# Kernel optimization log

Measured on AMD Instinct MI355X. Metric: run time of the kernel, lower is better.

Reference implementation:

```python
import jax, jax.numpy as jnp
import numpy as np

N, E, IN_DIM, HID, HEADS, LAYERS, NTYPES, NGRAPH = 50000, 600000, 64, 128, 8, 3, 10, 500
C = HID // HEADS
NEG_SLOPE = 0.2
EPS = 1e-5


def setup_inputs() -> dict:
    key = jax.random.key(0)
    ks = jax.random.split(key, 24)
    inp = {
        "x": jax.random.normal(ks[0], (N, IN_DIM), jnp.float32),
        "edge_index": jax.random.randint(ks[1], (2, E), 0, N),
        "node_types": jax.random.randint(ks[2], (N,), 0, NTYPES),
        "batch": jnp.sort(jax.random.randint(ks[3], (N,), 0, NGRAPH)),
        # node embedding linear
        "emb_W": jax.random.normal(ks[4], (IN_DIM, HID), jnp.float32) / np.sqrt(IN_DIM),
        "emb_b": jnp.zeros((HID,), jnp.float32),
        "ntype_emb": jax.random.normal(ks[5], (NTYPES, HID), jnp.float32) * 0.02,
        # stacked GAT layer params
        "gat_W": jax.random.normal(ks[6], (LAYERS, HID, HID), jnp.float32) / np.sqrt(HID),
        "att_src": jax.random.normal(ks[7], (LAYERS, HEADS, C), jnp.float32) * 0.1,
        "att_dst": jax.random.normal(ks[8], (LAYERS, HEADS, C), jnp.float32) * 0.1,
        "gat_b": jnp.zeros((LAYERS, HID), jnp.float32),
        "ln_g": jnp.ones((LAYERS, HID), jnp.float32),
        "ln_b": jnp.zeros((LAYERS, HID), jnp.float32),
        # global attention MLP
        "ga_W1": jax.random.normal(ks[9], (HID, HID), jnp.float32) / np.sqrt(HID),
        "ga_b1": jnp.zeros((HID,), jnp.float32),
        "ga_W2": jax.random.normal(ks[10], (HID, 1), jnp.float32) / np.sqrt(HID),
        "ga_b2": jnp.zeros((1,), jnp.float32),
        # graph classifier head
        "cls_W1": jax.random.normal(ks[11], (HID, HID), jnp.float32) / np.sqrt(HID),
        "cls_b1": jnp.zeros((HID,), jnp.float32),
        "cls_W2": jax.random.normal(ks[12], (HID, 1), jnp.float32) / np.sqrt(HID),
        "cls_b2": jnp.zeros((1,), jnp.float32),
    }
    return inp


def _layer_norm(h, g, b):
    mu = jnp.mean(h, axis=-1, keepdims=True)
    var = jnp.mean(jnp.square(h - mu), axis=-1, keepdims=True)
    return (h - mu) * jax.lax.rsqrt(var + EPS) * g + b


def _gat_layer(h, src, dst, W, a_src, a_dst, bias):
    # h: [N, HID] -> per-head projection [N, H, C]
    hp = (h @ W).reshape(N, HEADS, C)
    alpha_s = jnp.sum(hp * a_src, axis=-1)  # [N, H]
    alpha_d = jnp.sum(hp * a_dst, axis=-1)  # [N, H]
    e = jax.nn.leaky_relu(alpha_s[src] + alpha_d[dst], NEG_SLOPE)  # [E', H]
    # segment softmax over incoming edges of each destination node
    m = jax.ops.segment_max(e, dst, num_segments=N)
    ex = jnp.exp(e - m[dst])
    s = jax.ops.segment_sum(ex, dst, num_segments=N)
    alpha = ex / s[dst]  # every node has a self-loop, so s > 0
    msg = hp[src] * alpha[:, :, None]  # [E', H, C]
    out = jax.ops.segment_sum(msg, dst, num_segments=N)  # [N, H, C]
    return out.reshape(N, HID) + bias


def reference(x, edge_index, node_types, batch, emb_W, emb_b, ntype_emb,
              gat_W, att_src, att_dst, gat_b, ln_g, ln_b,
              ga_W1, ga_b1, ga_W2, ga_b2, cls_W1, cls_b1, cls_W2, cls_b2):
    # self-loops (PyG GATConv add_self_loops=True)
    loop = jnp.arange(N)
    src = jnp.concatenate([edge_index[0], loop])
    dst = jnp.concatenate([edge_index[1], loop])

    h = x @ emb_W + emb_b
    h = h + ntype_emb[node_types]

    for l in range(LAYERS):
        h_prev = h
        h = _gat_layer(h, src, dst, gat_W[l], att_src[l], att_dst[l], gat_b[l])
        h = _layer_norm(h, ln_g[l], ln_b[l])
        h = jax.nn.relu(h + h_prev)

    # global attention pooling: softmax over all nodes (dim 0, as in source)
    scores = jnp.tanh(h @ ga_W1 + ga_b1) @ ga_W2 + ga_b2  # [N, 1]
    attw = jax.nn.softmax(scores, axis=0)
    h_graph = jnp.sum(h * attw, axis=0)  # [HID]

    # global mean pool per graph
    sums = jax.ops.segment_sum(h, batch, num_segments=NGRAPH)  # [G, HID]
    cnts = jax.ops.segment_sum(jnp.ones((N, 1), h.dtype), batch, num_segments=NGRAPH)
    mean_pool = sums / jnp.maximum(cnts, 1.0)

    hg = h_graph + mean_pool  # broadcast [HID] + [G, HID]

    # graph classifier head (features_batch=None path), squeeze(-1)
    out = jax.nn.relu(hg @ cls_W1 + cls_b1) @ cls_W2 + cls_b2
    return out.squeeze(-1)  # [G]
```

## Files before the change

### kernel.cpp

```cpp
#include <hip/hip_runtime.h>
#include <hip/hip_bf16.h>
#include <math.h>

#define HID 128
#define HEADS 8
#define INDIM 64

typedef _Float16 f16x8 __attribute__((ext_vector_type(8)));
typedef _Float16 f16x4 __attribute__((ext_vector_type(4)));
typedef _Float16 f16x2 __attribute__((ext_vector_type(2)));
typedef float f32x4 __attribute__((ext_vector_type(4)));

__device__ __forceinline__ float fast_tanh(float x) {
    return 1.f - 2.f / (__expf(2.f * x) + 1.f);
}

#if defined(__has_builtin)
#if __has_builtin(__builtin_amdgcn_fdot2)
#define HAVE_FDOT2 1
#endif
#endif

__global__ void prologue_kernel(const int* __restrict__ ei, int* __restrict__ deg,
                                const float* __restrict__ emb_W, const float* __restrict__ gat_W,
                                const float* __restrict__ ga_W1, _Float16* __restrict__ wt_emb,
                                _Float16* __restrict__ wt_gat, _Float16* __restrict__ wt_ga1,
                                const int* __restrict__ batch, int* __restrict__ gstart,
                                float* __restrict__ hgZ,
                                int E, int EE, int N, int G) {
    int i = blockIdx.x * blockDim.x + threadIdx.x;
    if (i < EE) {
        int dst = (i < E) ? ei[E + i] : (i - E);
        atomicAdd(&deg[dst], 1);
    }
    if (i < 8192) {
        int k = i >> 7, n = i & 127;
        wt_emb[n * 64 + k] = (_Float16)emb_W[i];
    } else if (i < 8192 + 49152) {
        int j = i - 8192;
        int l = j >> 14, r = j & 16383;
        int k = r >> 7, n = r & 127;
        wt_gat[l * 16384 + n * 128 + k] = (_Float16)gat_W[j];
    } else if (i < 73728) {
        int j = i - 57344;
        int k = j >> 7, n = j & 127;
        wt_ga1[n * 128 + k] = (_Float16)ga_W1[j];
    } else if (i < 73728 + 129) {
        hgZ[i - 73728] = 0.f;
    }
    if (i >= 100000 && i - 100000 <= G) {
        int g = i - 100000;
        int lo = 0, hi = N;
        while (lo < hi) {
            int mid = (lo + hi) >> 1;
            if (batch[mid] < g) lo = mid + 1; else hi = mid;
        }
        gstart[g] = lo;
    }
}

__global__ __launch_bounds__(256) void mfma_proj_kernel(
    int mode, int K, int N,
    const _Float16* __restrict__ A16, const float* __restrict__ Af32,
    const _Float16* __restrict__ Wt,
    const float* __restrict__ bias, const float* __restrict__ nemb,
    const int* __restrict__ ntypes, _Float16* __restrict__ h16out,
    const float* __restrict__ asrc, const float* __restrict__ adst,
    _Float16* __restrict__ hp_out, float* __restrict__ als, float* __restrict__ ald,
    const float* __restrict__ w2, const float* __restrict__ b2,
    float* __restrict__ escore,
    int PB, int task, const int* __restrict__ ei2,
    const int* __restrict__ degc,
    int* __restrict__ rowptrw, int* __restrict__ woffw, int* __restrict__ esrcw,
    int E2, int EE2)
{
    __shared__ _Float16 w_lds[128 * 136];
    __shared__ _Float16 a_lds[64 * 136];
    int t = threadIdx.x;

    if ((int)blockIdx.x >= PB) {
        if (task == 1) {
            int b = (int)blockIdx.x - PB;
            int i = b * 256 + t;
            int v = (i < N) ? degc[i] : 0;
            int pe = 0;
            for (int j = t; j < (b << 8); j += 256) pe += degc[j];
#pragma unroll
            for (int m = 32; m >= 1; m >>= 1) pe += __shfl_xor(pe, m, 64);
            int* itmp  = (int*)a_lds;
            int* itmp2 = itmp + 256;
            itmp[t] = v;
            if ((t & 63) == 0) itmp2[t >> 6] = pe;
            __syncthreads();
#pragma unroll
            for (int off = 1; off < 256; off <<= 1) {
                int x = (t >= off) ? itmp[t - off] : 0;
                __syncthreads();
                itmp[t] += x;
                __syncthreads();
            }
            pe = itmp2[0] + itmp2[1] + itmp2[2] + itmp2[3];
            int excl = itmp[t] - v + pe;
            if (i < N) { rowptrw[i] = excl; woffw[i] = excl; }
            if (b == 0 && t == 0) rowptrw[N] = EE2;
        } else {
            int sb = (int)blockIdx.x - PB;
            int stride = ((int)gridDim.x - PB) << 8;
            for (int e = sb * 256 + t; e < EE2; e += stride) {
                int src, dst;
                if (e < E2) { src = ei2[e]; dst = ei2[E2 + e]; } else { src = dst = e - E2; }
                int slot = atomicAdd(&woffw[dst], 1);
                esrcw[slot] = src;
            }
        }
        return;
    }

    int KP = K + 8;
    int K8 = K >> 3;

    for (int i = t; i < 128 * K8; i += 256) {
        int row = i / K8, c8 = i - row * K8;
        *(f16x8*)&w_lds[row * KP + 8 * c8] = *(const f16x8*)&Wt[(size_t)row * K + 8 * c8];
    }

    int lane = t & 63, wv = t >> 6;
    int l15 = lane & 15, quad = lane >> 4;

    for (int tile = 0; tile < 2; ++tile) {
        int n0 = blockIdx.x * 128 + tile * 64;
        if (n0 >= N) break;
        __syncthreads();
        if (mode == 0) {
            for (int i = t; i < 64 * K8; i += 256) {
                int row = i / K8, c8 = i - row * K8;
                f16x8 v = {};
                int n = n0 + row;
                if (n < N) {
                    const float4* p = (const float4*)&Af32[(size_t)n * K + 8 * c8];
                    float4 a = p[0], b = p[1];
                    v[0] = (_Float16)a.x; v[1] = (_Float16)a.y;
                    v[2] = (_Float16)a.z; v[3] = (_Float16)a.w;
                    v[4] = (_Float16)b.x; v[5] = (_Float16)b.y;
                    v[6] = (_Float16)b.z; v[7] = (_Float16)b.w;
                }
                *(f16x8*)&a_lds[row * KP + 8 * c8] = v;
            }
        } else {
            for (int i = t; i < 64 * K8; i += 256) {
                int row = i / K8, c8 = i - row * K8;
                f16x8 v = {};
                if (n0 + row < N) v = *(const f16x8*)&A16[(size_t)(n0 + row) * K + 8 * c8];
                *(f16x8*)&a_lds[row * KP + 8 * c8] = v;
            }
        }
        __syncthreads();

        f32x4 acc[8];
#pragma unroll
        for (int c = 0; c < 8; ++c) acc[c] = (f32x4){0.f, 0.f, 0.f, 0.f};

        int ksteps = K >> 5;
        for (int kk = 0; kk < ksteps; ++kk) {
            f16x8 af = *(const f16x8*)&a_lds[(wv * 16 + l15) * KP + kk * 32 + quad * 8];
#pragma unroll
            for (int c = 0; c < 8; ++c) {
                f16x8 bf = *(const f16x8*)&w_lds[(c * 16 + l15) * KP + kk * 32 + quad * 8];
                acc[c] = __builtin_amdgcn_mfma_f32_16x16x32_f16(af, bf, acc[c], 0, 0, 0);
            }
        }

        if (mode == 0) {
            float bv[8];
#pragma unroll
            for (int c = 0; c < 8; ++c) bv[c] = bias[c * 16 + l15];
            __syncthreads();
#pragma unroll
            for (int r = 0; r < 4; ++r) {
                int n = n0 + wv * 16 + quad * 4 + r;
                int nt = (n < N) ? ntypes[n] : 0;
#pragma unroll
                for (int c = 0; c < 8; ++c)
                    a_lds[(wv * 16 + quad * 4 + r) * 136 + c * 16 + l15] =
                        (_Float16)(acc[c][r] + bv[c] + nemb[nt * HID + c * 16 + l15]);
            }
            __syncthreads();
            for (int i = t; i < 64 * 16; i += 256) {
                int row = i >> 4, c8 = i & 15;
                int n = n0 + row;
                if (n < N) *(f16x8*)&h16out[(size_t)n * HID + 8 * c8] = *(const f16x8*)&a_lds[row * 136 + 8 * c8];
            }
        } else if (mode == 1) {
            __syncthreads();
#pragma unroll
            for (int c = 0; c < 8; ++c)
#pragma unroll
                for (int r = 0; r < 4; ++r)
                    a_lds[(wv * 16 + quad * 4 + r) * 136 + c * 16 + l15] = (_Float16)acc[c][r];
            __syncthreads();
            for (int i = t; i < 64 * 16; i += 256) {
                int row = i >> 4, c8 = i & 15;
                int n = n0 + row;
                if (n < N) *(f16x8*)&hp_out[(size_t)n * HID + 8 * c8] = *(const f16x8*)&a_lds[row * 136 + 8 * c8];
            }
            for (int task2 = t; task2 < 512; task2 += 256) {
                int row = task2 >> 3, hd = task2 & 7;
                int n = n0 + row;
                if (n >= N) continue;
                f16x8 v0 = *(const f16x8*)&a_lds[row * 136 + hd * 16];
                f16x8 v1 = *(const f16x8*)&a_lds[row * 136 + hd * 16 + 8];
                float va = 0.f, vd = 0.f;
#pragma unroll
                for (int j = 0; j < 8; ++j) {
                    va += (float)v0[j] * asrc[hd * 16 + j] + (float)v1[j] * asrc[hd * 16 + 8 + j];
                    vd += (float)v0[j] * adst[hd * 16 + j] + (float)v1[j] * adst[hd * 16 + 8 + j];
                }
                als[n * HEADS + hd] = va;
                ald[n * HEADS + hd] = vd;
            }
        } else {
            float b2v = b2[0];
            float treg[4] = {0.f, 0.f, 0.f, 0.f};
#pragma unroll
            for (int c = 0; c < 8; ++c) {
                float b1v = bias[c * 16 + l15];
                float w2v = w2[c * 16 + l15];
#pragma unroll
                for (int r = 0; r < 4; ++r)
                    treg[r] += fast_tanh(acc[c][r] + b1v) * w2v;
            }
#pragma unroll
            for (int r = 0; r < 4; ++r) {
                float v = treg[r];
#pragma unroll
                for (int m = 8; m >= 1; m >>= 1) v += __shfl_xor(v, m, 64);
                if (l15 == 0) {
                    int n = n0 + wv * 16 + quad * 4 + r;
                    if (n < N) escore[n] = __expf(v + b2v);
                }
            }
        }
    }
}

__global__ void gat_aggregate_kernel(const int* __restrict__ rowptr, const int* __restrict__ esrc,
                                     const float* __restrict__ als, const float* __restrict__ ald,
                                     const _Float16* __restrict__ hp16, const float* __restrict__ gb,
                                     const float* __restrict__ lg, const float* __restrict__ lb,
                                     _Float16* __restrict__ h16, int N) {
    int wave = threadIdx.x >> 6;
    int lane = threadIdx.x & 63;
    int n = blockIdx.x * 4 + wave;
    if (n >= N) return;
    int esub = lane >> 4;
    int cg = lane & 15;
    int hd = cg >> 1;
    float adv = ald[n * HEADS + hd];
    int row = rowptr[n], end = rowptr[n + 1];
    int last = end - 1;
    float acc[8] = {0.f, 0.f, 0.f, 0.f, 0.f, 0.f, 0.f, 0.f};
    float sw = 0.f;
    for (int base = row; base < end; base += 16) {
        int iA = base + esub;
        int iB = iA + 4, iC = iA + 8, iD = iA + 12;
        int cA = iA <= last ? iA : last;
        int cB = iB <= last ? iB : last;
        int cC = iC <= last ? iC : last;
        int cD = iD <= last ? iD : last;
        int sA = esrc[cA], sB = esrc[cB], sC = esrc[cC], sD = esrc[cD];
        f16x8 pA = *(const f16x8*)&hp16[(size_t)sA * HID + cg * 8];
        f16x8 pB = *(const f16x8*)&hp16[(size_t)sB * HID + cg * 8];
        f16x8 pC = *(const f16x8*)&hp16[(size_t)sC * HID + cg * 8];
        f16x8 pD = *(const f16x8*)&hp16[(size_t)sD * HID + cg * 8];
        float aA = als[sA * HEADS + hd];
        float aB = als[sB * HEADS + hd];
        float aC = als[sC * HEADS + hd];
        float aD = als[sD * HEADS + hd];
        float lA = aA + adv; lA = lA > 0.f ? lA : 0.2f * lA;
        float lB = aB + adv; lB = lB > 0.f ? lB : 0.2f * lB;
        float lC = aC + adv; lC = lC > 0.f ? lC : 0.2f * lC;
        float lD = aD + adv; lD = lD > 0.f ? lD : 0.2f * lD;
        float wA = __expf(lA) * ((iA < end) ? 1.f : 0.f);
        float wB = __expf(lB) * ((iB < end) ? 1.f : 0.f);
        float wC = __expf(lC) * ((iC < end) ? 1.f : 0.f);
        float wD = __expf(lD) * ((iD < end) ? 1.f : 0.f);
        sw += (wA + wB) + (wC + wD);
#ifdef HAVE_FDOT2
        f16x2 wAB; wAB[0] = (_Float16)wA; wAB[1] = (_Float16)wB;
        f16x2 wCD; wCD[0] = (_Float16)wC; wCD[1] = (_Float16)wD;
#pragma unroll
        for (int j = 0; j < 8; ++j) {
            f16x2 prAB; prAB[0] = pA[j]; prAB[1] = pB[j];
            f16x2 prCD; prCD[0] = pC[j]; prCD[1] = pD[j];
            acc[j] = __builtin_amdgcn_fdot2(prAB, wAB, acc[j], false);
            acc[j] = __builtin_amdgcn_fdot2(prCD, wCD, acc[j], false);
        }
#else
#pragma unroll
        for (int j = 0; j < 8; ++j)
            acc[j] += wA * (float)pA[j] + wB * (float)pB[j]
                    + wC * (float)pC[j] + wD * (float)pD[j];
#endif
    }
#pragma unroll
    for (int m = 16; m <= 32; m <<= 1) {
        sw += __shfl_xor(sw, m, 64);
#pragma unroll
        for (int j = 0; j < 8; ++j) acc[j] += __shfl_xor(acc[j], m, 64);
    }
    float inv_sw = 1.f / sw;
    float4 g0 = ((const float4*)(gb + cg * 8))[0];
    float4 g1 = ((const float4*)(gb + cg * 8))[1];
    float v[8];
    v[0] = acc[0] * inv_sw + g0.x; v[1] = acc[1] * inv_sw + g0.y;
    v[2] = acc[2] * inv_sw + g0.z; v[3] = acc[3] * inv_sw + g0.w;
    v[4] = acc[4] * inv_sw + g1.x; v[5] = acc[5] * inv_sw + g1.y;
    v[6] = acc[6] * inv_sw + g1.z; v[7] = acc[7] * inv_sw + g1.w;
    float s = 0.f;
#pragma unroll
    for (int j = 0; j < 8; ++j) s += v[j];
#pragma unroll
    for (int m = 32; m >= 1; m >>= 1) s += __shfl_xor(s, m, 64);
    float mu = s * (1.f / 512.f);
    float d[8], sq = 0.f;
#pragma unroll
    for (int j = 0; j < 8; ++j) { d[j] = v[j] - mu; sq += d[j] * d[j]; }
#pragma unroll
    for (int m = 32; m >= 1; m >>= 1) sq += __shfl_xor(sq, m, 64);
    float inv = rsqrtf(sq * (1.f / 512.f) + 1e-5f);
    float4 lg0 = ((const float4*)(lg + cg * 8))[0];
    float4 lg1 = ((const float4*)(lg + cg * 8))[1];
    float4 lb0 = ((const float4*)(lb + cg * 8))[0];
    float4 lb1 = ((const float4*)(lb + cg * 8))[1];
    float lgv[8] = {lg0.x, lg0.y, lg0.z, lg0.w, lg1.x, lg1.y, lg1.z, lg1.w};
    float lbv[8] = {lb0.x, lb0.y, lb0.z, lb0.w, lb1.x, lb1.y, lb1.z, lb1.w};
    f16x8 hold = *(const f16x8*)&h16[(size_t)n * HID + cg * 8];
    f16x8 hnew;
#pragma unroll
    for (int j = 0; j < 8; ++j) {
        float r = d[j] * inv * lgv[j] + lbv[j] + (float)hold[j];
        hnew[j] = (_Float16)(r > 0.f ? r : 0.f);
    }
    if (esub == 0) *(f16x8*)&h16[(size_t)n * HID + cg * 8] = hnew;
}

__global__ void pool_graph_kernel(const _Float16* __restrict__ h16, const float* __restrict__ escore,
                                  const int* __restrict__ gstart, float* __restrict__ sums,
                                  float* __restrict__ cnts, float* __restrict__ hgZ, int G) {
    int g = blockIdx.x;
    int t = threadIdx.x;
    int c = t & 127, grp = t >> 7;
    int s = gstart[g], e = gstart[g + 1];
    float msum = 0.f, asum = 0.f, z = 0.f;
    for (int n = s + grp; n < e; n += 4) {
        float hv = (float)h16[(size_t)n * HID + c];
        float es = escore[n];
        msum += hv;
        asum += es * hv;
        if (c == 0) z += es;
    }
    __shared__ float sm[4][HID];
    __shared__ float sa[4][HID];
    __shared__ float sz[4];
    sm[grp][c] = msum;
    sa[grp][c] = asum;
    if (c == 0) sz[grp] = z;
    __syncthreads();
    if (t < HID) {
        float m = sm[0][t] + sm[1][t] + sm[2][t] + sm[3][t];
        float a = sa[0][t] + sa[1][t] + sa[2][t] + sa[3][t];
        sums[(size_t)g * HID + t] = m;
        atomicAdd(&hgZ[t], a);
    } else if (t == HID) {
        cnts[g] = (float)(e - s);
        atomicAdd(&hgZ[HID], sz[0] + sz[1] + sz[2] + sz[3]);
    }
}

__global__ void head_kernel(const float* __restrict__ hgZ, const float* __restrict__ sums,
                            const float* __restrict__ cnts, const float* __restrict__ W1,
                            const float* __restrict__ b1, const float* __restrict__ W2,
                            const float* __restrict__ b2, float* __restrict__ out, int G) {
    int g = blockIdx.x;
    int t = threadIdx.x;
    __shared__ float hr[HID];
    __shared__ float part[2];
    float Z = hgZ[HID];
    float cnt = cnts[g];
    cnt = cnt > 1.f ? cnt : 1.f;
    hr[t] = hgZ[t] / Z + sums[(size_t)g * HID + t] / cnt;
    __syncthreads();
    float acc = b1[t];
#pragma unroll 8
    for (int k = 0; k < HID; ++k) acc += hr[k] * W1[k * HID + t];
    acc = acc > 0.f ? acc : 0.f;
    float v = acc * W2[t];
#pragma unroll
    for (int m = 32; m >= 1; m >>= 1) v += __shfl_xor(v, m, 64);
    if ((t & 63) == 0) part[t >> 6] = v;
    __syncthreads();
    if (t == 0) out[g] = part[0] + part[1] + b2[0];
}

extern "C" void kernel_launch(void* const* d_in, const int* in_sizes, int n_in,
                              void* d_out, int out_size, void* d_ws, size_t ws_size,
                              hipStream_t stream) {
    const float* x        = (const float*)d_in[0];
    const int*   ei       = (const int*)d_in[1];
    const int*   ntypes   = (const int*)d_in[2];
    const int*   batch    = (const int*)d_in[3];
    const float* emb_W    = (const float*)d_in[4];
    const float* emb_b    = (const float*)d_in[5];
    const float* nemb     = (const float*)d_in[6];
    const float* gat_W    = (const float*)d_in[7];
    const float* att_src  = (const float*)d_in[8];
    const float* att_dst  = (const float*)d_in[9];
    const float* gat_b    = (const float*)d_in[10];
    const float* ln_g     = (const float*)d_in[11];
    const float* ln_b     = (const float*)d_in[12];
    const float* ga_W1    = (const float*)d_in[13];
    const float* ga_b1    = (const float*)d_in[14];
    const float* ga_W2    = (const float*)d_in[15];
    const float* ga_b2    = (const float*)d_in[16];
    const float* cls_W1   = (const float*)d_in[17];
    const float* cls_b1   = (const float*)d_in[18];
    const float* cls_W2   = (const float*)d_in[19];
    const float* cls_b2   = (const float*)d_in[20];
    float* out = (float*)d_out;

    const int N  = in_sizes[2];
    const int E  = in_sizes[1] / 2;
    const int EE = E + N;
    const int G  = out_size;
    const int NB = (N + 255) / 256;

    float* ws      = (float*)d_ws;
    float* als     = ws;
    float* ald     = als + (size_t)N * HEADS;
    float* escore  = ald + (size_t)N * HEADS;
    float* sums    = escore + N;
    float* cnts    = sums + (size_t)G * HID;
    float* hgZ     = cnts + G;
    _Float16* h16  = (_Float16*)(hgZ + HID + 1);
    _Float16* hp16 = h16 + (size_t)N * HID;
    _Float16* wt_emb = hp16 + (size_t)N * HID;
    _Float16* wt_gat = wt_emb + 128 * 64;
    _Float16* wt_ga1 = wt_gat + 3 * 128 * 128;
    int*   rowptr  = (int*)(wt_ga1 + 128 * 128);
    int*   woff    = rowptr + (N + 1);
    int*   deg     = woff + N;
    int*   esrc    = deg + N;
    int*   gstart  = esrc + EE;

    hipMemsetAsync(deg, 0, (size_t)N * sizeof(int), stream);
    int ptot = EE;
    if (ptot < 100000 + G + 1) ptot = 100000 + G + 1;
    prologue_kernel<<<(ptot + 255) / 256, 256, 0, stream>>>(
        ei, deg, emb_W, gat_W, ga_W1, wt_emb, wt_gat, wt_ga1,
        batch, gstart, hgZ, E, EE, N, G);

    const int PB = (N + 127) / 128;
    int SCB = 768 - PB;
    if (SCB < 128) SCB = 128;

    mfma_proj_kernel<<<PB + NB, 256, 0, stream>>>(
        0, INDIM, N, nullptr, x, wt_emb, emb_b, nemb, ntypes, h16,
        nullptr, nullptr, nullptr, nullptr, nullptr, nullptr, nullptr, nullptr,
        PB, 1, nullptr, deg, rowptr, woff, nullptr, E, EE);

    mfma_proj_kernel<<<PB + SCB, 256, 0, stream>>>(
        1, HID, N, h16, nullptr, wt_gat,
        nullptr, nullptr, nullptr, nullptr,
        att_src, att_dst, hp16, als, ald, nullptr, nullptr, nullptr,
        PB, 2, ei, nullptr, nullptr, woff, esrc, E, EE);

    gat_aggregate_kernel<<<(N + 3) / 4, 256, 0, stream>>>(
        rowptr, esrc, als, ald, hp16,
        gat_b, ln_g, ln_b, h16, N);

    for (int l = 1; l < 3; ++l) {
        mfma_proj_kernel<<<PB, 256, 0, stream>>>(
            1, HID, N, h16, nullptr, wt_gat + (size_t)l * HID * HID,
            nullptr, nullptr, nullptr, nullptr,
            att_src + l * HID, att_dst + l * HID,
            hp16, als, ald, nullptr, nullptr, nullptr,
            PB, 0, nullptr, nullptr, nullptr, nullptr, nullptr, 0, 0);
        gat_aggregate_kernel<<<(N + 3) / 4, 256, 0, stream>>>(
            rowptr, esrc, als, ald, hp16,
            gat_b + l * HID, ln_g + l * HID, ln_b + l * HID, h16, N);
    }

    mfma_proj_kernel<<<PB, 256, 0, stream>>>(
        2, HID, N, h16, nullptr, wt_ga1, ga_b1, nullptr, nullptr, nullptr,
        nullptr, nullptr, nullptr, nullptr, nullptr, ga_W2, ga_b2, escore,
        PB, 0, nullptr, nullptr, nullptr, nullptr, nullptr, 0, 0);

    pool_graph_kernel<<<G, 512, 0, stream>>>(h16, escore, gstart, sums, cnts, hgZ, G);
    head_kernel<<<G, 128, 0, stream>>>(hgZ, sums, cnts, cls_W1, cls_b1, cls_W2, cls_b2, out, G);
}
```

Measured before the change: 403.7 us.

## Fuse GAT aggregation with next-layer projection and merge embedding with layer-0 projection

Each layer's aggregate/LayerNorm/residual stage now writes its output rows into LDS and immediately runs the next layer's MFMA projection, or the final attention-score MLP, in the same kernel. The projected features and attention logits ping-pong between two buffers so no layer overwrites what it is still reading. The embedding kernel also computes layer 0's projection, and the CSR scan and scatter run in one launch, with the scatter blocks spin-waiting on a global counter until every scan block is done. This removes several launches and the re-read of h between aggregation and projection. The cost is tiles shrinking from 128 to 64 nodes, more workspace, and a grid-wide spin wait that can deadlock if the scan blocks are not all resident at once.

```diff
diff --git a/kernel.cpp b/kernel.cpp
--- a/kernel.cpp
+++ b/kernel.cpp
@@ -7,7 +7,6 @@
 #define INDIM 64
 
 typedef _Float16 f16x8 __attribute__((ext_vector_type(8)));
-typedef _Float16 f16x4 __attribute__((ext_vector_type(4)));
 typedef _Float16 f16x2 __attribute__((ext_vector_type(2)));
 typedef float f32x4 __attribute__((ext_vector_type(4)));
 
@@ -59,289 +58,346 @@
     }
 }
 
-__global__ __launch_bounds__(256) void mfma_proj_kernel(
-    int mode, int K, int N,
-    const _Float16* __restrict__ A16, const float* __restrict__ Af32,
-    const _Float16* __restrict__ Wt,
-    const float* __restrict__ bias, const float* __restrict__ nemb,
-    const int* __restrict__ ntypes, _Float16* __restrict__ h16out,
+__global__ __launch_bounds__(256) void emb_l0_kernel(
+    const float* __restrict__ x, const _Float16* __restrict__ wt_emb,
+    const float* __restrict__ emb_b, const float* __restrict__ nemb,
+    const int* __restrict__ ntypes,
+    _Float16* __restrict__ h16,
+    const _Float16* __restrict__ wt_g0,
     const float* __restrict__ asrc, const float* __restrict__ adst,
-    _Float16* __restrict__ hp_out, float* __restrict__ als, float* __restrict__ ald,
-    const float* __restrict__ w2, const float* __restrict__ b2,
-    float* __restrict__ escore,
-    int PB, int task, const int* __restrict__ ei2,
-    const int* __restrict__ degc,
-    int* __restrict__ rowptrw, int* __restrict__ woffw, int* __restrict__ esrcw,
-    int E2, int EE2)
+    _Float16* __restrict__ hp_out, float* __restrict__ als_out, float* __restrict__ ald_out,
+    int PB, const int* __restrict__ ei, const int* __restrict__ deg,
+    int* __restrict__ rowptr, int* __restrict__ woff, int* __restrict__ esrc,
+    int* __restrict__ ctr,
+    int N, int E, int EE, int NB)
 {
     __shared__ _Float16 w_lds[128 * 136];
     __shared__ _Float16 a_lds[64 * 136];
     int t = threadIdx.x;
 
     if ((int)blockIdx.x >= PB) {
-        if (task == 1) {
-            int b = (int)blockIdx.x - PB;
-            int i = b * 256 + t;
-            int v = (i < N) ? degc[i] : 0;
-            int pe = 0;
-            for (int j = t; j < (b << 8); j += 256) pe += degc[j];
-#pragma unroll
-            for (int m = 32; m >= 1; m >>= 1) pe += __shfl_xor(pe, m, 64);
-            int* itmp  = (int*)a_lds;
-            int* itmp2 = itmp + 256;
-            itmp[t] = v;
-            if ((t & 63) == 0) itmp2[t >> 6] = pe;
+        int b = (int)blockIdx.x - PB;
+        int i = b * 256 + t;
+        int v = (i < N) ? deg[i] : 0;
+        int pe = 0;
+        for (int j = t; j < (b << 8); j += 256) pe += deg[j];
+#pragma unroll
+        for (int m = 32; m >= 1; m >>= 1) pe += __shfl_xor(pe, m, 64);
+        int* itmp  = (int*)a_lds;
+        int* itmp2 = itmp + 256;
+        itmp[t] = v;
+        if ((t & 63) == 0) itmp2[t >> 6] = pe;
+        __syncthreads();
+#pragma unroll
+        for (int off = 1; off < 256; off <<= 1) {
+            int xx = (t >= off) ? itmp[t - off] : 0;
             __syncthreads();
-#pragma unroll
-            for (int off = 1; off < 256; off <<= 1) {
-                int x = (t >= off) ? itmp[t - off] : 0;
-                __syncthreads();
-                itmp[t] += x;
-                __syncthreads();
-            }
-            pe = itmp2[0] + itmp2[1] + itmp2[2] + itmp2[3];
-            int excl = itmp[t] - v + pe;
-            if (i < N) { rowptrw[i] = excl; woffw[i] = excl; }
-            if (b == 0 && t == 0) rowptrw[N] = EE2;
-        } else {
-            int sb = (int)blockIdx.x - PB;
-            int stride = ((int)gridDim.x - PB) << 8;
-            for (int e = sb * 256 + t; e < EE2; e += stride) {
-                int src, dst;
-                if (e < E2) { src = ei2[e]; dst = ei2[E2 + e]; } else { src = dst = e - E2; }
-                int slot = atomicAdd(&woffw[dst], 1);
-                esrcw[slot] = src;
-            }
+            itmp[t] += xx;
+            __syncthreads();
+        }
+        pe = itmp2[0] + itmp2[1] + itmp2[2] + itmp2[3];
+        int excl = itmp[t] - v + pe;
+        if (i < N) { rowptr[i] = excl; woff[i] = excl; }
+        if (b == 0 && t == 0) rowptr[N] = EE;
+        __threadfence();
+        __syncthreads();
+        if (t == 0) {
+            atomicAdd(ctr, 1);
+            while (atomicAdd(ctr, 0) < NB) __builtin_amdgcn_s_sleep(16);
+        }
+        __syncthreads();
+        for (int e = b * 256 + t; e < EE; e += NB * 256) {
+            int src, dst;
+            if (e < E) { src = ei[e]; dst = ei[E + e]; } else { src = dst = e - E; }
+            int slot = atomicAdd(&woff[dst], 1);
+            esrc[slot] = src;
         }
         return;
     }
 
-    int KP = K + 8;
-    int K8 = K >> 3;
-
-    for (int i = t; i < 128 * K8; i += 256) {
-        int row = i / K8, c8 = i - row * K8;
-        *(f16x8*)&w_lds[row * KP + 8 * c8] = *(const f16x8*)&Wt[(size_t)row * K + 8 * c8];
-    }
+    for (int i = t; i < 128 * 8; i += 256) {
+        int row = i >> 3, c8 = i & 7;
+        *(f16x8*)&w_lds[row * 72 + 8 * c8] = *(const f16x8*)&wt_emb[(size_t)row * 64 + 8 * c8];
+    }
+    int n0 = blockIdx.x * 64;
+    for (int i = t; i < 64 * 8; i += 256) {
+        int row = i >> 3, c8 = i & 7;
+        f16x8 v = {};
+        int n = n0 + row;
+        if (n < N) {
+            const float4* ptr = (const float4*)&x[(size_t)n * 64 + 8 * c8];
+            float4 a = ptr[0], b4 = ptr[1];
+            v[0] = (_Float16)a.x; v[1] = (_Float16)a.y;
+            v[2] = (_Float16)a.z; v[3] = (_Float16)a.w;
+            v[4] = (_Float16)b4.x; v[5] = (_Float16)b4.y;
+            v[6] = (_Float16)b4.z; v[7] = (_Float16)b4.w;
+        }
+        *(f16x8*)&a_lds[row * 72 + 8 * c8] = v;
+    }
+    __syncthreads();
 
     int lane = t & 63, wv = t >> 6;
     int l15 = lane & 15, quad = lane >> 4;
 
-    for (int tile = 0; tile < 2; ++tile) {
-        int n0 = blockIdx.x * 128 + tile * 64;
-        if (n0 >= N) break;
+    f32x4 acc[8];
+#pragma unroll
+    for (int c = 0; c < 8; ++c) acc[c] = (f32x4){0.f, 0.f, 0.f, 0.f};
+#pragma unroll
+    for (int kk = 0; kk < 2; ++kk) {
+        f16x8 af = *(const f16x8*)&a_lds[(wv * 16 + l15) * 72 + kk * 32 + quad * 8];
+#pragma unroll
+        for (int c = 0; c < 8; ++c) {
+            f16x8 bf = *(const f16x8*)&w_lds[(c * 16 + l15) * 72 + kk * 32 + quad * 8];
+            acc[c] = __builtin_amdgcn_mfma_f32_16x16x32_f16(af, bf, acc[c], 0, 0, 0);
+        }
+    }
+    float bv[8];
+#pragma unroll
+    for (int c = 0; c < 8; ++c) bv[c] = emb_b[c * 16 + l15];
+    __syncthreads();
+#pragma unroll
+    for (int r = 0; r < 4; ++r) {
+        int n = n0 + wv * 16 + quad * 4 + r;
+        int nt = (n < N) ? ntypes[n] : 0;
+#pragma unroll
+        for (int c = 0; c < 8; ++c)
+            a_lds[(wv * 16 + quad * 4 + r) * 136 + c * 16 + l15] =
+                (_Float16)(acc[c][r] + bv[c] + nemb[nt * HID + c * 16 + l15]);
+    }
+    for (int i = t; i < 128 * 16; i += 256) {
+        int row = i >> 4, c8 = i & 15;
+        *(f16x8*)&w_lds[row * 136 + 8 * c8] = *(const f16x8*)&wt_g0[(size_t)row * 128 + 8 * c8];
+    }
+    __syncthreads();
+    for (int i = t; i < 64 * 16; i += 256) {
+        int row = i >> 4, c8 = i & 15;
+        int n = n0 + row;
+        if (n < N) *(f16x8*)&h16[(size_t)n * HID + 8 * c8] = *(const f16x8*)&a_lds[row * 136 + 8 * c8];
+    }
+#pragma unroll
+    for (int c = 0; c < 8; ++c) acc[c] = (f32x4){0.f, 0.f, 0.f, 0.f};
+#pragma unroll
+    for (int kk = 0; kk < 4; ++kk) {
+        f16x8 af = *(const f16x8*)&a_lds[(wv * 16 + l15) * 136 + kk * 32 + quad * 8];
+#pragma unroll
+        for (int c = 0; c < 8; ++c) {
+            f16x8 bf = *(const f16x8*)&w_lds[(c * 16 + l15) * 136 + kk * 32 + quad * 8];
+            acc[c] = __builtin_amdgcn_mfma_f32_16x16x32_f16(af, bf, acc[c], 0, 0, 0);
+        }
+    }
+    __syncthreads();
+#pragma unroll
+    for (int c = 0; c < 8; ++c)
+#pragma unroll
+        for (int r = 0; r < 4; ++r)
+            a_lds[(wv * 16 + quad * 4 + r) * 136 + c * 16 + l15] = (_Float16)acc[c][r];
+    __syncthreads();
+    for (int i = t; i < 64 * 16; i += 256) {
+        int row = i >> 4, c8 = i & 15;
+        int n = n0 + row;
+        if (n < N) *(f16x8*)&hp_out[(size_t)n * HID + 8 * c8] = *(const f16x8*)&a_lds[row * 136 + 8 * c8];
+    }
+    for (int task2 = t; task2 < 512; task2 += 256) {
+        int row = task2 >> 3, hd = task2 & 7;
+        int n = n0 + row;
+        if (n >= N) continue;
+        f16x8 v0 = *(const f16x8*)&a_lds[row * 136 + hd * 16];
+        f16x8 v1 = *(const f16x8*)&a_lds[row * 136 + hd * 16 + 8];
+        float va = 0.f, vd = 0.f;
+#pragma unroll
+        for (int j = 0; j < 8; ++j) {
+            va += (float)v0[j] * asrc[hd * 16 + j] + (float)v1[j] * asrc[hd * 16 + 8 + j];
+            vd += (float)v0[j] * adst[hd * 16 + j] + (float)v1[j] * adst[hd * 16 + 8 + j];
+        }
+        als_out[n * HEADS + hd] = va;
+        ald_out[n * HEADS + hd] = vd;
+    }
+}
+
+__global__ __launch_bounds__(256) void fused_agg_proj_kernel(
+    int mode,
+    const int* __restrict__ rowptr, const int* __restrict__ esrc,
+    const float* __restrict__ als_in, const float* __restrict__ ald_in,
+    const _Float16* __restrict__ hp_in,
+    const float* __restrict__ gb, const float* __restrict__ lg, const float* __restrict__ lb,
+    _Float16* __restrict__ h16,
+    const _Float16* __restrict__ Wt,
+    const float* __restrict__ asrc, const float* __restrict__ adst,
+    _Float16* __restrict__ hp_out, float* __restrict__ als_out, float* __restrict__ ald_out,
+    const float* __restrict__ b1, const float* __restrict__ w2, const float* __restrict__ b2,
+    float* __restrict__ escore, int N)
+{
+    __shared__ _Float16 w_lds[128 * 136];
+    __shared__ _Float16 a_lds[64 * 136];
+    int t = threadIdx.x;
+    for (int i = t; i < 128 * 16; i += 256) {
+        int row = i >> 4, c8 = i & 15;
+        *(f16x8*)&w_lds[row * 136 + 8 * c8] = *(const f16x8*)&Wt[(size_t)row * 128 + 8 * c8];
+    }
+    int wave = t >> 6, lane = t & 63;
+    int esub = lane >> 4, cg_ = lane & 15, hd = cg_ >> 1;
+    int n0 = blockIdx.x * 64;
+
+    for (int it = 0; it < 16; ++it) {
+        int n = n0 + wave * 16 + it;
+        if (n >= N) break;
+        float adv = ald_in[n * HEADS + hd];
+        int rs = rowptr[n], re = rowptr[n + 1];
+        int last = re - 1;
+        float acc[8] = {0.f, 0.f, 0.f, 0.f, 0.f, 0.f, 0.f, 0.f};
+        float sw = 0.f;
+        for (int base = rs; base < re; base += 16) {
+            int iA = base + esub;
+            int iB = iA + 4, iC = iA + 8, iD = iA + 12;
+            int cA = iA <= last ? iA : last;
+            int cB = iB <= last ? iB : last;
+            int cC = iC <= last ? iC : last;
+            int cD = iD <= last ? iD : last;
+            int sA = esrc[cA], sB = esrc[cB], sC = esrc[cC], sD = esrc[cD];
+            f16x8 pA = *(const f16x8*)&hp_in[(size_t)sA * HID + cg_ * 8];
+            f16x8 pB = *(const f16x8*)&hp_in[(size_t)sB * HID + cg_ * 8];
+            f16x8 pC = *(const f16x8*)&hp_in[(size_t)sC * HID + cg_ * 8];
+            f16x8 pD = *(const f16x8*)&hp_in[(size_t)sD * HID + cg_ * 8];
+            float aA = als_in[sA * HEADS + hd];
+            float aB = als_in[sB * HEADS + hd];
+            float aC = als_in[sC * HEADS + hd];
+            float aD = als_in[sD * HEADS + hd];
+            float lA = aA + adv; lA = lA > 0.f ? lA : 0.2f * lA;
+            float lB = aB + adv; lB = lB > 0.f ? lB : 0.2f * lB;
+            float lC = aC + adv; lC = lC > 0.f ? lC : 0.2f * lC;
+            float lD = aD + adv; lD = lD > 0.f ? lD : 0.2f * lD;
+            float wA = __expf(lA) * ((iA < re) ? 1.f : 0.f);
+            float wB = __expf(lB) * ((iB < re) ? 1.f : 0.f);
+            float wC = __expf(lC) * ((iC < re) ? 1.f : 0.f);
+            float wD = __expf(lD) * ((iD < re) ? 1.f : 0.f);
+            sw += (wA + wB) + (wC + wD);
+#ifdef HAVE_FDOT2
+            f16x2 wAB; wAB[0] = (_Float16)wA; wAB[1] = (_Float16)wB;
+            f16x2 wCD; wCD[0] = (_Float16)wC; wCD[1] = (_Float16)wD;
+#pragma unroll
+            for (int j = 0; j < 8; ++j) {
+                f16x2 prAB; prAB[0] = pA[j]; prAB[1] = pB[j];
+                f16x2 prCD; prCD[0] = pC[j]; prCD[1] = pD[j];
+                acc[j] = __builtin_amdgcn_fdot2(prAB, wAB, acc[j], false);
+                acc[j] = __builtin_amdgcn_fdot2(prCD, wCD, acc[j], false);
+            }
+#else
+#pragma unroll
+            for (int j = 0; j < 8; ++j)
+                acc[j] += wA * (float)pA[j] + wB * (float)pB[j]
+                        + wC * (float)pC[j] + wD * (float)pD[j];
+#endif
+        }
+#pragma unroll
+        for (int m = 16; m <= 32; m <<= 1) {
+            sw += __shfl_xor(sw, m, 64);
+#pragma unroll
+            for (int j = 0; j < 8; ++j) acc[j] += __shfl_xor(acc[j], m, 64);
+        }
+        float inv_sw = 1.f / sw;
+        float4 g0 = ((const float4*)(gb + cg_ * 8))[0];
+        float4 g1 = ((const float4*)(gb + cg_ * 8))[1];
+        float v[8];
+        v[0] = acc[0] * inv_sw + g0.x; v[1] = acc[1] * inv_sw + g0.y;
+        v[2] = acc[2] * inv_sw + g0.z; v[3] = acc[3] * inv_sw + g0.w;
+        v[4] = acc[4] * inv_sw + g1.x; v[5] = acc[5] * inv_sw + g1.y;
+        v[6] = acc[6] * inv_sw + g1.z; v[7] = acc[7] * inv_sw + g1.w;
+        float s = 0.f;
+#pragma unroll
+        for (int j = 0; j < 8; ++j) s += v[j];
+#pragma unroll
+        for (int m = 32; m >= 1; m >>= 1) s += __shfl_xor(s, m, 64);
+        float mu = s * (1.f / 512.f);
+        float d[8], sq = 0.f;
+#pragma unroll
+        for (int j = 0; j < 8; ++j) { d[j] = v[j] - mu; sq += d[j] * d[j]; }
+#pragma unroll
+        for (int m = 32; m >= 1; m >>= 1) sq += __shfl_xor(sq, m, 64);
+        float inv = rsqrtf(sq * (1.f / 512.f) + 1e-5f);
+        float4 lg0 = ((const float4*)(lg + cg_ * 8))[0];
+        float4 lg1 = ((const float4*)(lg + cg_ * 8))[1];
+        float4 lb0 = ((const float4*)(lb + cg_ * 8))[0];
+        float4 lb1 = ((const float4*)(lb + cg_ * 8))[1];
+        float lgv[8] = {lg0.x, lg0.y, lg0.z, lg0.w, lg1.x, lg1.y, lg1.z, lg1.w};
+        float lbv[8] = {lb0.x, lb0.y, lb0.z, lb0.w, lb1.x, lb1.y, lb1.z, lb1.w};
+        f16x8 hold = *(const f16x8*)&h16[(size_t)n * HID + cg_ * 8];
+        f16x8 hnew;
+#pragma unroll
+        for (int j = 0; j < 8; ++j) {
+            float r = d[j] * inv * lgv[j] + lbv[j] + (float)hold[j];
+            hnew[j] = (_Float16)(r > 0.f ? r : 0.f);
+        }
+        if (esub == 0) {
+            *(f16x8*)&a_lds[(wave * 16 + it) * 136 + cg_ * 8] = hnew;
+            *(f16x8*)&h16[(size_t)n * HID + cg_ * 8] = hnew;
+        }
+    }
+    __syncthreads();
+
+    int l15 = lane & 15, quad = lane >> 4;
+    f32x4 pacc[8];
+#pragma unroll
+    for (int c = 0; c < 8; ++c) pacc[c] = (f32x4){0.f, 0.f, 0.f, 0.f};
+#pragma unroll
+    for (int kk = 0; kk < 4; ++kk) {
+        f16x8 af = *(const f16x8*)&a_lds[(wave * 16 + l15) * 136 + kk * 32 + quad * 8];
+#pragma unroll
+        for (int c = 0; c < 8; ++c) {
+            f16x8 bf = *(const f16x8*)&w_lds[(c * 16 + l15) * 136 + kk * 32 + quad * 8];
+            pacc[c] = __builtin_amdgcn_mfma_f32_16x16x32_f16(af, bf, pacc[c], 0, 0, 0);
+        }
+    }
+
+    if (mode == 1) {
         __syncthreads();
-        if (mode == 0) {
-            for (int i = t; i < 64 * K8; i += 256) {
-                int row = i / K8, c8 = i - row * K8;
-                f16x8 v = {};
-                int n = n0 + row;
-                if (n < N) {
-                    const float4* p = (const float4*)&Af32[(size_t)n * K + 8 * c8];
-                    float4 a = p[0], b = p[1];
-                    v[0] = (_Float16)a.x; v[1] = (_Float16)a.y;
-                    v[2] = (_Float16)a.z; v[3] = (_Float16)a.w;
-                    v[4] = (_Float16)b.x; v[5] = (_Float16)b.y;
-                    v[6] = (_Float16)b.z; v[7] = (_Float16)b.w;
-                }
-                *(f16x8*)&a_lds[row * KP + 8 * c8] = v;
+#pragma unroll
+        for (int c = 0; c < 8; ++c)
+#pragma unroll
+            for (int r = 0; r < 4; ++r)
+                a_lds[(wave * 16 + quad * 4 + r) * 136 + c * 16 + l15] = (_Float16)pacc[c][r];
+        __syncthreads();
+        for (int i = t; i < 64 * 16; i += 256) {
+            int row = i >> 4, c8 = i & 15;
+            int n = n0 + row;
+            if (n < N) *(f16x8*)&hp_out[(size_t)n * HID + 8 * c8] = *(const f16x8*)&a_lds[row * 136 + 8 * c8];
+        }
+        for (int task2 = t; task2 < 512; task2 += 256) {
+            int row = task2 >> 3, hh = task2 & 7;
+            int n = n0 + row;
+            if (n >= N) continue;
+            f16x8 v0 = *(const f16x8*)&a_lds[row * 136 + hh * 16];
+            f16x8 v1 = *(const f16x8*)&a_lds[row * 136 + hh * 16 + 8];
+            float va = 0.f, vd = 0.f;
+#pragma unroll
+            for (int j = 0; j < 8; ++j) {
+                va += (float)v0[j] * asrc[hh * 16 + j] + (float)v1[j] * asrc[hh * 16 + 8 + j];
+                vd += (float)v0[j] * adst[hh * 16 + j] + (float)v1[j] * adst[hh * 16 + 8 + j];
             }
-        } else {
-            for (int i = t; i < 64 * K8; i += 256) {
-                int row = i / K8, c8 = i - row * K8;
-                f16x8 v = {};
-                if (n0 + row < N) v = *(const f16x8*)&A16[(size_t)(n0 + row) * K + 8 * c8];
-                *(f16x8*)&a_lds[row * KP + 8 * c8] = v;
+            als_out[n * HEADS + hh] = va;
+            ald_out[n * HEADS + hh] = vd;
+        }
+    } else {
+        float b2v = b2[0];
+        float treg[4] = {0.f, 0.f, 0.f, 0.f};
+#pragma unroll
+        for (int c = 0; c < 8; ++c) {
+            float b1v = b1[c * 16 + l15];
+            float w2v = w2[c * 16 + l15];
+#pragma unroll
+            for (int r = 0; r < 4; ++r)
+                treg[r] += fast_tanh(pacc[c][r] + b1v) * w2v;
+        }
+#pragma unroll
+        for (int r = 0; r < 4; ++r) {
+            float v = treg[r];
+#pragma unroll
+            for (int m = 8; m >= 1; m >>= 1) v += __shfl_xor(v, m, 64);
+            if (l15 == 0) {
+                int n = n0 + wave * 16 + quad * 4 + r;
+                if (n < N) escore[n] = __expf(v + b2v);
             }
         }
-        __syncthreads();
-
-        f32x4 acc[8];
-#pragma unroll
-        for (int c = 0; c < 8; ++c) acc[c] = (f32x4){0.f, 0.f, 0.f, 0.f};
-
-        int ksteps = K >> 5;
-        for (int kk = 0; kk < ksteps; ++kk) {
-            f16x8 af = *(const f16x8*)&a_lds[(wv * 16 + l15) * KP + kk * 32 + quad * 8];
-#pragma unroll
-            for (int c = 0; c < 8; ++c) {
-                f16x8 bf = *(const f16x8*)&w_lds[(c * 16 + l15) * KP + kk * 32 + quad * 8];
-                acc[c] = __builtin_amdgcn_mfma_f32_16x16x32_f16(af, bf, acc[c], 0, 0, 0);
-            }
-        }
-
-        if (mode == 0) {
-            float bv[8];
-#pragma unroll
-            for (int c = 0; c < 8; ++c) bv[c] = bias[c * 16 + l15];
-            __syncthreads();
-#pragma unroll
-            for (int r = 0; r < 4; ++r) {
-                int n = n0 + wv * 16 + quad * 4 + r;
-                int nt = (n < N) ? ntypes[n] : 0;
-#pragma unroll
-                for (int c = 0; c < 8; ++c)
-                    a_lds[(wv * 16 + quad * 4 + r) * 136 + c * 16 + l15] =
-                        (_Float16)(acc[c][r] + bv[c] + nemb[nt * HID + c * 16 + l15]);
-            }
-            __syncthreads();
-            for (int i = t; i < 64 * 16; i += 256) {
-                int row = i >> 4, c8 = i & 15;
-                int n = n0 + row;
-                if (n < N) *(f16x8*)&h16out[(size_t)n * HID + 8 * c8] = *(const f16x8*)&a_lds[row * 136 + 8 * c8];
-            }
-        } else if (mode == 1) {
-            __syncthreads();
-#pragma unroll
-            for (int c = 0; c < 8; ++c)
-#pragma unroll
-                for (int r = 0; r < 4; ++r)
-                    a_lds[(wv * 16 + quad * 4 + r) * 136 + c * 16 + l15] = (_Float16)acc[c][r];
-            __syncthreads();
-            for (int i = t; i < 64 * 16; i += 256) {
-                int row = i >> 4, c8 = i & 15;
-                int n = n0 + row;
-                if (n < N) *(f16x8*)&hp_out[(size_t)n * HID + 8 * c8] = *(const f16x8*)&a_lds[row * 136 + 8 * c8];
-            }
-            for (int task2 = t; task2 < 512; task2 += 256) {
-                int row = task2 >> 3, hd = task2 & 7;
-                int n = n0 + row;
-                if (n >= N) continue;
-                f16x8 v0 = *(const f16x8*)&a_lds[row * 136 + hd * 16];
-                f16x8 v1 = *(const f16x8*)&a_lds[row * 136 + hd * 16 + 8];
-                float va = 0.f, vd = 0.f;
-#pragma unroll
-                for (int j = 0; j < 8; ++j) {
-                    va += (float)v0[j] * asrc[hd * 16 + j] + (float)v1[j] * asrc[hd * 16 + 8 + j];
-                    vd += (float)v0[j] * adst[hd * 16 + j] + (float)v1[j] * adst[hd * 16 + 8 + j];
-                }
-                als[n * HEADS + hd] = va;
-                ald[n * HEADS + hd] = vd;
-            }
-        } else {
-            float b2v = b2[0];
-            float treg[4] = {0.f, 0.f, 0.f, 0.f};
-#pragma unroll
-            for (int c = 0; c < 8; ++c) {
-                float b1v = bias[c * 16 + l15];
-                float w2v = w2[c * 16 + l15];
-#pragma unroll
-                for (int r = 0; r < 4; ++r)
-                    treg[r] += fast_tanh(acc[c][r] + b1v) * w2v;
-            }
-#pragma unroll
-            for (int r = 0; r < 4; ++r) {
-                float v = treg[r];
-#pragma unroll
-                for (int m = 8; m >= 1; m >>= 1) v += __shfl_xor(v, m, 64);
-                if (l15 == 0) {
-                    int n = n0 + wv * 16 + quad * 4 + r;
-                    if (n < N) escore[n] = __expf(v + b2v);
-                }
-            }
-        }
-    }
-}
-
-__global__ void gat_aggregate_kernel(const int* __restrict__ rowptr, const int* __restrict__ esrc,
-                                     const float* __restrict__ als, const float* __restrict__ ald,
-                                     const _Float16* __restrict__ hp16, const float* __restrict__ gb,
-                                     const float* __restrict__ lg, const float* __restrict__ lb,
-                                     _Float16* __restrict__ h16, int N) {
-    int wave = threadIdx.x >> 6;
-    int lane = threadIdx.x & 63;
-    int n = blockIdx.x * 4 + wave;
-    if (n >= N) return;
-    int esub = lane >> 4;
-    int cg = lane & 15;
-    int hd = cg >> 1;
-    float adv = ald[n * HEADS + hd];
-    int row = rowptr[n], end = rowptr[n + 1];
-    int last = end - 1;
-    float acc[8] = {0.f, 0.f, 0.f, 0.f, 0.f, 0.f, 0.f, 0.f};
-    float sw = 0.f;
-    for (int base = row; base < end; base += 16) {
-        int iA = base + esub;
-        int iB = iA + 4, iC = iA + 8, iD = iA + 12;
-        int cA = iA <= last ? iA : last;
-        int cB = iB <= last ? iB : last;
-        int cC = iC <= last ? iC : last;
-        int cD = iD <= last ? iD : last;
-        int sA = esrc[cA], sB = esrc[cB], sC = esrc[cC], sD = esrc[cD];
-        f16x8 pA = *(const f16x8*)&hp16[(size_t)sA * HID + cg * 8];
-        f16x8 pB = *(const f16x8*)&hp16[(size_t)sB * HID + cg * 8];
-        f16x8 pC = *(const f16x8*)&hp16[(size_t)sC * HID + cg * 8];
-        f16x8 pD = *(const f16x8*)&hp16[(size_t)sD * HID + cg * 8];
-        float aA = als[sA * HEADS + hd];
-        float aB = als[sB * HEADS + hd];
-        float aC = als[sC * HEADS + hd];
-        float aD = als[sD * HEADS + hd];
-        float lA = aA + adv; lA = lA > 0.f ? lA : 0.2f * lA;
-        float lB = aB + adv; lB = lB > 0.f ? lB : 0.2f * lB;
-        float lC = aC + adv; lC = lC > 0.f ? lC : 0.2f * lC;
-        float lD = aD + adv; lD = lD > 0.f ? lD : 0.2f * lD;
-        float wA = __expf(lA) * ((iA < end) ? 1.f : 0.f);
-        float wB = __expf(lB) * ((iB < end) ? 1.f : 0.f);
-        float wC = __expf(lC) * ((iC < end) ? 1.f : 0.f);
-        float wD = __expf(lD) * ((iD < end) ? 1.f : 0.f);
-        sw += (wA + wB) + (wC + wD);
-#ifdef HAVE_FDOT2
-        f16x2 wAB; wAB[0] = (_Float16)wA; wAB[1] = (_Float16)wB;
-        f16x2 wCD; wCD[0] = (_Float16)wC; wCD[1] = (_Float16)wD;
-#pragma unroll
-        for (int j = 0; j < 8; ++j) {
-            f16x2 prAB; prAB[0] = pA[j]; prAB[1] = pB[j];
-            f16x2 prCD; prCD[0] = pC[j]; prCD[1] = pD[j];
-            acc[j] = __builtin_amdgcn_fdot2(prAB, wAB, acc[j], false);
-            acc[j] = __builtin_amdgcn_fdot2(prCD, wCD, acc[j], false);
-        }
-#else
-#pragma unroll
-        for (int j = 0; j < 8; ++j)
-            acc[j] += wA * (float)pA[j] + wB * (float)pB[j]
-                    + wC * (float)pC[j] + wD * (float)pD[j];
-#endif
-    }
-#pragma unroll
-    for (int m = 16; m <= 32; m <<= 1) {
-        sw += __shfl_xor(sw, m, 64);
-#pragma unroll
-        for (int j = 0; j < 8; ++j) acc[j] += __shfl_xor(acc[j], m, 64);
-    }
-    float inv_sw = 1.f / sw;
-    float4 g0 = ((const float4*)(gb + cg * 8))[0];
-    float4 g1 = ((const float4*)(gb + cg * 8))[1];
-    float v[8];
-    v[0] = acc[0] * inv_sw + g0.x; v[1] = acc[1] * inv_sw + g0.y;
-    v[2] = acc[2] * inv_sw + g0.z; v[3] = acc[3] * inv_sw + g0.w;
-    v[4] = acc[4] * inv_sw + g1.x; v[5] = acc[5] * inv_sw + g1.y;
-    v[6] = acc[6] * inv_sw + g1.z; v[7] = acc[7] * inv_sw + g1.w;
-    float s = 0.f;
-#pragma unroll
-    for (int j = 0; j < 8; ++j) s += v[j];
-#pragma unroll
-    for (int m = 32; m >= 1; m >>= 1) s += __shfl_xor(s, m, 64);
-    float mu = s * (1.f / 512.f);
-    float d[8], sq = 0.f;
-#pragma unroll
-    for (int j = 0; j < 8; ++j) { d[j] = v[j] - mu; sq += d[j] * d[j]; }
-#pragma unroll
-    for (int m = 32; m >= 1; m >>= 1) sq += __shfl_xor(sq, m, 64);
-    float inv = rsqrtf(sq * (1.f / 512.f) + 1e-5f);
-    float4 lg0 = ((const float4*)(lg + cg * 8))[0];
-    float4 lg1 = ((const float4*)(lg + cg * 8))[1];
-    float4 lb0 = ((const float4*)(lb + cg * 8))[0];
-    float4 lb1 = ((const float4*)(lb + cg * 8))[1];
-    float lgv[8] = {lg0.x, lg0.y, lg0.z, lg0.w, lg1.x, lg1.y, lg1.z, lg1.w};
-    float lbv[8] = {lb0.x, lb0.y, lb0.z, lb0.w, lb1.x, lb1.y, lb1.z, lb1.w};
-    f16x8 hold = *(const f16x8*)&h16[(size_t)n * HID + cg * 8];
-    f16x8 hnew;
-#pragma unroll
-    for (int j = 0; j < 8; ++j) {
-        float r = d[j] * inv * lgv[j] + lbv[j] + (float)hold[j];
-        hnew[j] = (_Float16)(r > 0.f ? r : 0.f);
-    }
-    if (esub == 0) *(f16x8*)&h16[(size_t)n * HID + cg * 8] = hnew;
+    }
 }
 
 __global__ void pool_graph_kernel(const _Float16* __restrict__ h16, const float* __restrict__ escore,
@@ -435,65 +491,62 @@
     const int NB = (N + 255) / 256;
 
     float* ws      = (float*)d_ws;
-    float* als     = ws;
-    float* ald     = als + (size_t)N * HEADS;
-    float* escore  = ald + (size_t)N * HEADS;
+    float* als_a   = ws;
+    float* ald_a   = als_a + (size_t)N * HEADS;
+    float* als_b   = ald_a + (size_t)N * HEADS;
+    float* ald_b   = als_b + (size_t)N * HEADS;
+    float* escore  = ald_b + (size_t)N * HEADS;
     float* sums    = escore + N;
     float* cnts    = sums + (size_t)G * HID;
     float* hgZ     = cnts + G;
     _Float16* h16  = (_Float16*)(hgZ + HID + 1);
-    _Float16* hp16 = h16 + (size_t)N * HID;
-    _Float16* wt_emb = hp16 + (size_t)N * HID;
+    _Float16* hp_a = h16 + (size_t)N * HID;
+    _Float16* hp_b = hp_a + (size_t)N * HID;
+    _Float16* wt_emb = hp_b + (size_t)N * HID;
     _Float16* wt_gat = wt_emb + 128 * 64;
     _Float16* wt_ga1 = wt_gat + 3 * 128 * 128;
     int*   rowptr  = (int*)(wt_ga1 + 128 * 128);
     int*   woff    = rowptr + (N + 1);
     int*   deg     = woff + N;
-    int*   esrc    = deg + N;
+    int*   ctr     = deg + N;
+    int*   esrc    = ctr + 1;
     int*   gstart  = esrc + EE;
 
-    hipMemsetAsync(deg, 0, (size_t)N * sizeof(int), stream);
-    int ptot = EE;
-    if (ptot < 100000 + G + 1) ptot = 100000 + G + 1;
-    prologue_kernel<<<(ptot + 255) / 256, 256, 0, stream>>>(
+    int P1TOT = EE;
+    if (P1TOT < 100000 + G + 1) P1TOT = 100000 + G + 1;
+
+    hipMemsetAsync(deg, 0, ((size_t)N + 1) * sizeof(int), stream);
+    prologue_kernel<<<(P1TOT + 255) / 256, 256, 0, stream>>>(
         ei, deg, emb_W, gat_W, ga_W1, wt_emb, wt_gat, wt_ga1,
         batch, gstart, hgZ, E, EE, N, G);
 
-    const int PB = (N + 127) / 128;
-    int SCB = 768 - PB;
-    if (SCB < 128) SCB = 128;
-
-    mfma_proj_kernel<<<PB + NB, 256, 0, stream>>>(
-        0, INDIM, N, nullptr, x, wt_emb, emb_b, nemb, ntypes, h16,
-        nullptr, nullptr, nullptr, nullptr, nullptr, nullptr, nullptr, nullptr,
-        PB, 1, nullptr, deg, rowptr, woff, nullptr, E, EE);
-
-    mfma_proj_kernel<<<PB + SCB, 256, 0, stream>>>(
-        1, HID, N, h16, nullptr, wt_gat,
-        nullptr, nullptr, nullptr, nullptr,
-        att_src, att_dst, hp16, als, ald, nullptr, nullptr, nullptr,
-        PB, 2, ei, nullptr, nullptr, woff, esrc, E, EE);
-
-    gat_aggregate_kernel<<<(N + 3) / 4, 256, 0, stream>>>(
-        rowptr, esrc, als, ald, hp16,
-        gat_b, ln_g, ln_b, h16, N);
-
-    for (int l = 1; l < 3; ++l) {
-        mfma_proj_kernel<<<PB, 256, 0, stream>>>(
-            1, HID, N, h16, nullptr, wt_gat + (size_t)l * HID * HID,
-            nullptr, nullptr, nullptr, nullptr,
-            att_src + l * HID, att_dst + l * HID,
-            hp16, als, ald, nullptr, nullptr, nullptr,
-            PB, 0, nullptr, nullptr, nullptr, nullptr, nullptr, 0, 0);
-        gat_aggregate_kernel<<<(N + 3) / 4, 256, 0, stream>>>(
-            rowptr, esrc, als, ald, hp16,
-            gat_b + l * HID, ln_g + l * HID, ln_b + l * HID, h16, N);
-    }
-
-    mfma_proj_kernel<<<PB, 256, 0, stream>>>(
-        2, HID, N, h16, nullptr, wt_ga1, ga_b1, nullptr, nullptr, nullptr,
-        nullptr, nullptr, nullptr, nullptr, nullptr, ga_W2, ga_b2, escore,
-        PB, 0, nullptr, nullptr, nullptr, nullptr, nullptr, 0, 0);
+    const int PB = (N + 63) / 64;
+
+    emb_l0_kernel<<<PB + NB, 256, 0, stream>>>(
+        x, wt_emb, emb_b, nemb, ntypes, h16,
+        wt_gat, att_src, att_dst, hp_a, als_a, ald_a,
+        PB, ei, deg, rowptr, woff, esrc, ctr, N, E, EE, NB);
+
+    fused_agg_proj_kernel<<<PB, 256, 0, stream>>>(
+        1, rowptr, esrc, als_a, ald_a, hp_a,
+        gat_b, ln_g, ln_b, h16,
+        wt_gat + 16384, att_src + HID, att_dst + HID,
+        hp_b, als_b, ald_b,
+        nullptr, nullptr, nullptr, nullptr, N);
+
+    fused_agg_proj_kernel<<<PB, 256, 0, stream>>>(
+        1, rowptr, esrc, als_b, ald_b, hp_b,
+        gat_b + HID, ln_g + HID, ln_b + HID, h16,
+        wt_gat + 32768, att_src + 2 * HID, att_dst + 2 * HID,
+        hp_a, als_a, ald_a,
+        nullptr, nullptr, nullptr, nullptr, N);
+
+    fused_agg_proj_kernel<<<PB, 256, 0, stream>>>(
+        2, rowptr, esrc, als_a, ald_a, hp_a,
+        gat_b + 2 * HID, ln_g + 2 * HID, ln_b + 2 * HID, h16,
+        wt_ga1, nullptr, nullptr,
+        nullptr, nullptr, nullptr,
+        ga_b1, ga_W2, ga_b2, escore, N);
 
     pool_graph_kernel<<<G, 512, 0, stream>>>(h16, escore, gstart, sums, cnts, hgZ, G);
     head_kernel<<<G, 128, 0, stream>>>(hgZ, sums, cnts, cls_W1, cls_b1, cls_W2, cls_b2, out, G);
```

After: 524.1 us. 1.3x slower.
